# Optimization experiments

Measured on AMD Instinct MI355X. Metric: run time of the kernel, lower is better.

## Reference

```python
import jax, jax.numpy as jnp
import numpy as np
import math

N_NODES = 100000
N_EDGES = 1600000
INPUT_SIZE = 256
N_HEADS = 8
HEAD_SIZE = INPUT_SIZE // N_HEADS  # 32
DK = math.sqrt(HEAD_SIZE)


def setup_inputs() -> dict:
    key = jax.random.key(0)
    k1, k2, k3, k4, k5 = jax.random.split(key, 5)
    X = jax.random.normal(k1, (N_NODES, INPUT_SIZE), dtype=jnp.float32)
    edge_index = jax.random.randint(k2, (2, N_EDGES), 0, N_NODES, dtype=jnp.int64)
    # kaiming_normal (fan_in = input_size) std = sqrt(2/fan_in)
    std = math.sqrt(2.0 / INPUT_SIZE)
    Wq = jax.random.normal(k3, (INPUT_SIZE, HEAD_SIZE), dtype=jnp.float32) * std
    Wk = jax.random.normal(k4, (INPUT_SIZE, HEAD_SIZE), dtype=jnp.float32) * std
    Wv = jax.random.normal(k5, (INPUT_SIZE, HEAD_SIZE), dtype=jnp.float32) * std
    return {"X": X, "edge_index": edge_index, "Wq": Wq, "Wk": Wk, "Wv": Wv}


def reference(X, edge_index, Wq, Wk, Wv):
    N = X.shape[0]
    Q = X @ Wq  # [N, h]
    K = X @ Wk  # [N, h]
    V = X @ Wv  # [N, h]
    src = edge_index[0]  # row index (softmax over dim=1 -> per-src segments)
    dst = edge_index[1]
    # per-edge QK dot, scaled
    scores = jnp.sum(Q[src] * K[dst], axis=-1) / DK  # [E]
    # segment-wise (sparse) softmax over each row
    row_max = jax.ops.segment_max(scores, src, num_segments=N)  # [N]
    ex = jnp.exp(scores - row_max[src])  # [E]
    denom = jax.ops.segment_sum(ex, src, num_segments=N)  # [N]
    alpha = ex / denom[src]  # [E]
    # sparse-mm aggregate of V: out[i] = sum_j alpha_ij * V[j]
    out = jax.ops.segment_sum(alpha[:, None] * V[dst], src, num_segments=N)  # [N, h]
    return out
```

## Files before the change

### kernel.cpp

```cpp
#include <hip/hip_runtime.h>

#define N_INPUT 256
#define HS 32

#define BKT_SHIFT 7
#define BKT_NODES 128
#define NBUCK_MAX 800
#define CAP 2560
#define EPB 2048

typedef __attribute__((ext_vector_type(8))) short bf16x8;
typedef __attribute__((ext_vector_type(4))) float f32x4;
typedef __attribute__((ext_vector_type(8))) unsigned short u16x8;

__device__ __forceinline__ unsigned short f2bf(float f) {
    unsigned u = __float_as_uint(f);
    unsigned r = u + 0x7FFFu + ((u >> 16) & 1u);
    return (unsigned short)(r >> 16);
}
__device__ __forceinline__ float bf2f(unsigned short u) {
    return __uint_as_float((unsigned)u << 16);
}

__global__ void prep_kernel(int* __restrict__ gtail, int nb,
                            const float* __restrict__ Wq,
                            const float* __restrict__ Wk,
                            const float* __restrict__ Wv,
                            uint4* __restrict__ Wp) {
    int t = threadIdx.x;
    if (blockIdx.x == 0) {
        for (int i = t; i < nb; i += 256) gtail[i] = 0;
        return;
    }
    int c = (int)(blockIdx.x - 1) * 256 + t;
    int s = c >> 9;
    int tt = (c >> 6) & 7;
    int L = c & 63;
    const float* wm = (s < 2) ? Wq : (s < 4) ? Wk : Wv;
    const float* wsrc = wm + (size_t)(tt * 32 + (L >> 4) * 8) * HS + (s & 1) * 16 + (L & 15);
    unsigned e0 = f2bf(wsrc[0 * HS]) | ((unsigned)f2bf(wsrc[1 * HS]) << 16);
    unsigned e1 = f2bf(wsrc[2 * HS]) | ((unsigned)f2bf(wsrc[3 * HS]) << 16);
    unsigned e2 = f2bf(wsrc[4 * HS]) | ((unsigned)f2bf(wsrc[5 * HS]) << 16);
    unsigned e3 = f2bf(wsrc[6 * HS]) | ((unsigned)f2bf(wsrc[7 * HS]) << 16);
    Wp[c] = make_uint4(e0, e1, e2, e3);
}

__global__ __launch_bounds__(256) void mega_kernel(
        const float* __restrict__ X, const uint4* __restrict__ Wp,
        const int* __restrict__ src, const int* __restrict__ dst,
        float* __restrict__ Q, unsigned short* __restrict__ KVb,
        int* __restrict__ gtail, uint2* __restrict__ staging,
        int N, int E, int nb, int s1blocks) {
    __shared__ int sh[NBUCK_MAX];
    __shared__ int sbs[NBUCK_MAX];
    int tid = threadIdx.x;
    int idx = (int)blockIdx.x;
    bool is_s1 = (idx % 3 == 0) && (idx / 3 < s1blocks);

    if (is_s1) {
        int e0 = (idx / 3) * EPB;
        for (int i = tid; i < nb; i += 256) sh[i] = 0;
        __syncthreads();
        int ss[8], dd[8], rr[8];
#pragma unroll
        for (int k = 0; k < 8; ++k) {
            int i = e0 + tid + k * 256;
            ss[k] = -1;
            if (i < E) {
                int s = src[i];
                dd[k] = dst[i];
                ss[k] = s;
                rr[k] = atomicAdd(&sh[s >> BKT_SHIFT], 1);
            }
        }
        __syncthreads();
        for (int b = tid; b < nb; b += 256) {
            int c = sh[b];
            sbs[b] = c ? atomicAdd(&gtail[b], c) : 0;
        }
        __syncthreads();
#pragma unroll
        for (int k = 0; k < 8; ++k) {
            if (ss[k] >= 0) {
                int b = ss[k] >> BKT_SHIFT;
                int pos = sbs[b] + rr[k];
                if (pos < CAP)
                    staging[(size_t)b * CAP + pos] =
                        make_uint2((unsigned)ss[k], (unsigned)dd[k]);
            }
        }
        return;
    }

    int bq = idx - min(idx / 3 + 1, s1blocks);
    int wave = tid >> 6;
    int L = tid & 63;
    int quad = L >> 4;
    int lane16 = L & 15;
    int mt = bq * 4 + wave;
    if (mt * 16 >= N) return;

    const float* xrow = X + (size_t)(mt * 16 + lane16) * N_INPUT + quad * 8;
    bf16x8 afrag[8];
#pragma unroll
    for (int t = 0; t < 8; ++t) {
        float4 a0 = *(const float4*)(xrow + t * 32);
        float4 a1 = *(const float4*)(xrow + t * 32 + 4);
        bf16x8 f;
        f[0] = (short)f2bf(a0.x); f[1] = (short)f2bf(a0.y);
        f[2] = (short)f2bf(a0.z); f[3] = (short)f2bf(a0.w);
        f[4] = (short)f2bf(a1.x); f[5] = (short)f2bf(a1.y);
        f[6] = (short)f2bf(a1.z); f[7] = (short)f2bf(a1.w);
        afrag[t] = f;
    }

#pragma unroll
    for (int s = 0; s < 6; ++s) {
        f32x4 acc = {0.f, 0.f, 0.f, 0.f};
#pragma unroll
        for (int t = 0; t < 8; ++t) {
            bf16x8 bfrag = ((const bf16x8*)Wp)[(s * 8 + t) * 64 + L];
            acc = __builtin_amdgcn_mfma_f32_16x16x32_bf16(afrag[t], bfrag, acc, 0, 0, 0);
        }
        int col = (s & 1) * 16 + lane16;
#pragma unroll
        for (int r = 0; r < 4; ++r) {
            int row = mt * 16 + quad * 4 + r;
            if (s < 2) {
                Q[(size_t)row * HS + col] = acc[r];
            } else {
                size_t pos = (size_t)row * 64 + (size_t)(col >> 2) * 8 +
                             ((s < 4) ? 0 : 4) + (col & 3);
                KVb[pos] = f2bf(acc[r]);
            }
        }
    }
}

__global__ __launch_bounds__(512) void s2_agg_kernel(
        const uint2* __restrict__ staging, const int* __restrict__ gtail,
        const float* __restrict__ Q, const unsigned short* __restrict__ KVb,
        float* __restrict__ out, int N) {
    __shared__ int ldst[CAP];
    __shared__ int nh[BKT_NODES];
    __shared__ int nx[BKT_NODES];
    __shared__ int rk[BKT_NODES];
    int b = blockIdx.x;
    int t = threadIdx.x;
    int cnt = min(gtail[b], CAP);
    if (t < BKT_NODES) { nh[t] = 0; rk[t] = 0; }
    __syncthreads();
    uint2 stash[5];
#pragma unroll
    for (int k = 0; k < 5; ++k) {
        int i = t + k * 512;
        if (i < cnt) {
            uint2 e = staging[(size_t)b * CAP + i];
            stash[k] = e;
            atomicAdd(&nh[e.x & (BKT_NODES - 1)], 1);
        }
    }
    __syncthreads();
    if (t < BKT_NODES) nx[t] = nh[t];
    __syncthreads();
    for (int off = 1; off < BKT_NODES; off <<= 1) {
        int u = (t >= off && t < BKT_NODES) ? nx[t - off] : 0;
        __syncthreads();
        if (t < BKT_NODES) nx[t] += u;
        __syncthreads();
    }
#pragma unroll
    for (int k = 0; k < 5; ++k) {
        int i = t + k * 512;
        if (i < cnt) {
            uint2 e = stash[k];
            int sl = (int)(e.x & (BKT_NODES - 1));
            int r = atomicAdd(&rk[sl], 1);
            ldst[nx[sl] - nh[sl] + r] = (int)e.y;
        }
    }
    __syncthreads();

    int lane = t & 31;
    int grp = t >> 5;
    int slot = lane >> 3;
    int sub = lane & 7;
    int node0 = b << BKT_SHIFT;
    for (int ni = grp; ni < BKT_NODES; ni += 16) {
        int n = node0 + ni;
        if (n >= N) continue;
        int end = nx[ni];
        int beg = end - nh[ni];
        float4 qf = *(const float4*)(Q + (size_t)n * HS + sub * 4);
        float4 acc = make_float4(0.f, 0.f, 0.f, 0.f);
        float den = 0.f;
        for (int j = beg; j < end; j += 4) {
            int e = j + slot;
            bool valid = e < end;
            int d = valid ? ldst[e] : 0;
            u16x8 kv = *(const u16x8*)(KVb + (size_t)d * 64 + sub * 8);
            float p = qf.x * bf2f(kv[0]) + qf.y * bf2f(kv[1]) +
                      qf.z * bf2f(kv[2]) + qf.w * bf2f(kv[3]);
            p += __shfl_xor(p, 1, 32);
            p += __shfl_xor(p, 2, 32);
            p += __shfl_xor(p, 4, 32);
            float ex = valid ? __expf(p * 0.17677669529663687f) : 0.f;
            den += ex;
            acc.x += ex * bf2f(kv[4]);
            acc.y += ex * bf2f(kv[5]);
            acc.z += ex * bf2f(kv[6]);
            acc.w += ex * bf2f(kv[7]);
        }
#pragma unroll
        for (int off = 8; off <= 16; off <<= 1) {
            acc.x += __shfl_xor(acc.x, off, 32);
            acc.y += __shfl_xor(acc.y, off, 32);
            acc.z += __shfl_xor(acc.z, off, 32);
            acc.w += __shfl_xor(acc.w, off, 32);
            den += __shfl_xor(den, off, 32);
        }
        if (lane < 8) {
            float4 o = make_float4(0.f, 0.f, 0.f, 0.f);
            if (end > beg) {
                float rd = 1.f / den;
                o = make_float4(acc.x * rd, acc.y * rd, acc.z * rd, acc.w * rd);
            }
            *(float4*)(out + (size_t)n * HS + lane * 4) = o;
        }
    }
}

extern "C" void kernel_launch(void* const* d_in, const int* in_sizes, int n_in,
                              void* d_out, int out_size, void* d_ws, size_t ws_size,
                              hipStream_t stream) {
    const float* X  = (const float*)d_in[0];
    const int*   ei = (const int*)d_in[1];
    const float* Wq = (const float*)d_in[2];
    const float* Wk = (const float*)d_in[3];
    const float* Wv = (const float*)d_in[4];

    int N = in_sizes[0] / N_INPUT;
    int E = in_sizes[1] / 2;
    const int* src = ei;
    const int* dst = ei + E;

    float* ws = (float*)d_ws;
    float* Q = ws;
    unsigned short* KVb = (unsigned short*)(Q + (size_t)N * HS);
    uint4* Wp = (uint4*)(KVb + (size_t)N * 64);
    int* gtail = (int*)(Wp + 3072);
    uint2* staging = (uint2*)(gtail + NBUCK_MAX);
    float* out = (float*)d_out;

    int nbuck = (N + BKT_NODES - 1) >> BKT_SHIFT;
    int s1blocks = (E + EPB - 1) / EPB;
    int mtiles = (N + 15) / 16;
    int qblocks = (mtiles + 3) / 4;

    prep_kernel<<<13, 256, 0, stream>>>(gtail, nbuck, Wq, Wk, Wv, Wp);
    mega_kernel<<<s1blocks + qblocks, 256, 0, stream>>>(
        X, Wp, src, dst, Q, KVb, gtail, staging, N, E, nbuck, s1blocks);
    s2_agg_kernel<<<nbuck, 512, 0, stream>>>(staging, gtail, Q, KVb, out, N);
}
```

Baseline: 231.8 us.

## Pack staged edges into 32-bit words and enlarge binning chunks per block

Staged edges are now packed into one 32-bit word holding the local source slot (7 bits) and the destination index (17 bits) instead of an 8-byte pair. This halves staging write and read traffic between the binning and aggregation stages. Each binning block now processes 16384 edges with a two-pass count-then-scatter loop, which cuts the number of global gtail atomics. The interleave ratio between binning and projection blocks is now computed from the block counts. The cost is that src is read twice and fewer, longer binning blocks may finish late. The packing also limits node indices to 17 bits, which only holds for N up to 131072.

```diff
diff --git a/kernel.cpp b/kernel.cpp
--- a/kernel.cpp
+++ b/kernel.cpp
@@ -7,7 +7,7 @@
 #define BKT_NODES 128
 #define NBUCK_MAX 800
 #define CAP 2560
-#define EPB 2048
+#define EPB 16384
 
 typedef __attribute__((ext_vector_type(8))) short bf16x8;
 typedef __attribute__((ext_vector_type(4))) float f32x4;
@@ -49,50 +49,42 @@
         const float* __restrict__ X, const uint4* __restrict__ Wp,
         const int* __restrict__ src, const int* __restrict__ dst,
         float* __restrict__ Q, unsigned short* __restrict__ KVb,
-        int* __restrict__ gtail, uint2* __restrict__ staging,
-        int N, int E, int nb, int s1blocks) {
+        int* __restrict__ gtail, unsigned* __restrict__ staging,
+        int N, int E, int nb, int s1blocks, int ilv) {
     __shared__ int sh[NBUCK_MAX];
     __shared__ int sbs[NBUCK_MAX];
+    __shared__ int srk[NBUCK_MAX];
     int tid = threadIdx.x;
     int idx = (int)blockIdx.x;
-    bool is_s1 = (idx % 3 == 0) && (idx / 3 < s1blocks);
+    bool is_s1 = (idx % ilv == 0) && (idx / ilv < s1blocks);
 
     if (is_s1) {
-        int e0 = (idx / 3) * EPB;
-        for (int i = tid; i < nb; i += 256) sh[i] = 0;
-        __syncthreads();
-        int ss[8], dd[8], rr[8];
-#pragma unroll
-        for (int k = 0; k < 8; ++k) {
-            int i = e0 + tid + k * 256;
-            ss[k] = -1;
-            if (i < E) {
-                int s = src[i];
-                dd[k] = dst[i];
-                ss[k] = s;
-                rr[k] = atomicAdd(&sh[s >> BKT_SHIFT], 1);
-            }
-        }
+        int e0 = (idx / ilv) * EPB;
+        int lim = min(EPB, E - e0);
+        for (int i = tid; i < nb; i += 256) { sh[i] = 0; srk[i] = 0; }
+        __syncthreads();
+        for (int i = tid; i < lim; i += 256)
+            atomicAdd(&sh[src[e0 + i] >> BKT_SHIFT], 1);
         __syncthreads();
         for (int b = tid; b < nb; b += 256) {
             int c = sh[b];
             sbs[b] = c ? atomicAdd(&gtail[b], c) : 0;
         }
         __syncthreads();
-#pragma unroll
-        for (int k = 0; k < 8; ++k) {
-            if (ss[k] >= 0) {
-                int b = ss[k] >> BKT_SHIFT;
-                int pos = sbs[b] + rr[k];
-                if (pos < CAP)
-                    staging[(size_t)b * CAP + pos] =
-                        make_uint2((unsigned)ss[k], (unsigned)dd[k]);
-            }
+        for (int i = tid; i < lim; i += 256) {
+            int s = src[e0 + i];
+            unsigned d = (unsigned)dst[e0 + i];
+            int b = s >> BKT_SHIFT;
+            int r = atomicAdd(&srk[b], 1);
+            int pos = sbs[b] + r;
+            if (pos < CAP)
+                staging[(size_t)b * CAP + pos] =
+                    ((unsigned)(s & (BKT_NODES - 1)) << 17) | d;
         }
         return;
     }
 
-    int bq = idx - min(idx / 3 + 1, s1blocks);
+    int bq = idx - min(idx / ilv + 1, s1blocks);
     int wave = tid >> 6;
     int L = tid & 63;
     int quad = L >> 4;
@@ -138,7 +130,7 @@
 }
 
 __global__ __launch_bounds__(512) void s2_agg_kernel(
-        const uint2* __restrict__ staging, const int* __restrict__ gtail,
+        const unsigned* __restrict__ staging, const int* __restrict__ gtail,
         const float* __restrict__ Q, const unsigned short* __restrict__ KVb,
         float* __restrict__ out, int N) {
     __shared__ int ldst[CAP];
@@ -150,14 +142,14 @@
     int cnt = min(gtail[b], CAP);
     if (t < BKT_NODES) { nh[t] = 0; rk[t] = 0; }
     __syncthreads();
-    uint2 stash[5];
+    unsigned stash[5];
 #pragma unroll
     for (int k = 0; k < 5; ++k) {
         int i = t + k * 512;
         if (i < cnt) {
-            uint2 e = staging[(size_t)b * CAP + i];
+            unsigned e = staging[(size_t)b * CAP + i];
             stash[k] = e;
-            atomicAdd(&nh[e.x & (BKT_NODES - 1)], 1);
+            atomicAdd(&nh[e >> 17], 1);
         }
     }
     __syncthreads();
@@ -173,10 +165,10 @@
     for (int k = 0; k < 5; ++k) {
         int i = t + k * 512;
         if (i < cnt) {
-            uint2 e = stash[k];
-            int sl = (int)(e.x & (BKT_NODES - 1));
+            unsigned e = stash[k];
+            int sl = (int)(e >> 17);
             int r = atomicAdd(&rk[sl], 1);
-            ldst[nx[sl] - nh[sl] + r] = (int)e.y;
+            ldst[nx[sl] - nh[sl] + r] = (int)(e & 0x1FFFFu);
         }
     }
     __syncthreads();
@@ -249,16 +241,19 @@
     unsigned short* KVb = (unsigned short*)(Q + (size_t)N * HS);
     uint4* Wp = (uint4*)(KVb + (size_t)N * 64);
     int* gtail = (int*)(Wp + 3072);
-    uint2* staging = (uint2*)(gtail + NBUCK_MAX);
+    unsigned* staging = (unsigned*)(gtail + NBUCK_MAX);
     float* out = (float*)d_out;
 
     int nbuck = (N + BKT_NODES - 1) >> BKT_SHIFT;
     int s1blocks = (E + EPB - 1) / EPB;
     int mtiles = (N + 15) / 16;
     int qblocks = (mtiles + 3) / 4;
+    int total = s1blocks + qblocks;
+    int ilv = total / s1blocks;
+    if (ilv < 1) ilv = 1;
 
     prep_kernel<<<13, 256, 0, stream>>>(gtail, nbuck, Wq, Wk, Wv, Wp);
-    mega_kernel<<<s1blocks + qblocks, 256, 0, stream>>>(
-        X, Wp, src, dst, Q, KVb, gtail, staging, N, E, nbuck, s1blocks);
+    mega_kernel<<<total, 256, 0, stream>>>(
+        X, Wp, src, dst, Q, KVb, gtail, staging, N, E, nbuck, s1blocks, ilv);
     s2_agg_kernel<<<nbuck, 512, 0, stream>>>(staging, gtail, Q, KVb, out, N);
 }
```

New measurement: 472.8 us. +103.9%, slower.

## Pack staged edges into 32-bit words and prefetch next KV gather

Applied to the files above, without the earlier changes.

Staging entries drop from a (src,dst) uint2 to a single 32-bit word holding the local source slot (7 bits) and the destination (17 bits). This halves the staging write and read traffic between the bucketing and aggregation kernels. The aggregation loop also software-pipelines the gathered KV load, fetching the next iteration's row while the current one is being computed, to hide gather latency. The packing assumes fewer than 2^17 nodes, and the prefetch adds register pressure.

```diff
diff --git a/kernel.cpp b/kernel.cpp
--- a/kernel.cpp
+++ b/kernel.cpp
@@ -49,7 +49,7 @@
         const float* __restrict__ X, const uint4* __restrict__ Wp,
         const int* __restrict__ src, const int* __restrict__ dst,
         float* __restrict__ Q, unsigned short* __restrict__ KVb,
-        int* __restrict__ gtail, uint2* __restrict__ staging,
+        int* __restrict__ gtail, unsigned* __restrict__ staging,
         int N, int E, int nb, int s1blocks) {
     __shared__ int sh[NBUCK_MAX];
     __shared__ int sbs[NBUCK_MAX];
@@ -86,7 +86,7 @@
                 int pos = sbs[b] + rr[k];
                 if (pos < CAP)
                     staging[(size_t)b * CAP + pos] =
-                        make_uint2((unsigned)ss[k], (unsigned)dd[k]);
+                        ((unsigned)(ss[k] & (BKT_NODES - 1)) << 17) | (unsigned)dd[k];
             }
         }
         return;
@@ -138,7 +138,7 @@
 }
 
 __global__ __launch_bounds__(512) void s2_agg_kernel(
-        const uint2* __restrict__ staging, const int* __restrict__ gtail,
+        const unsigned* __restrict__ staging, const int* __restrict__ gtail,
         const float* __restrict__ Q, const unsigned short* __restrict__ KVb,
         float* __restrict__ out, int N) {
     __shared__ int ldst[CAP];
@@ -150,14 +150,14 @@
     int cnt = min(gtail[b], CAP);
     if (t < BKT_NODES) { nh[t] = 0; rk[t] = 0; }
     __syncthreads();
-    uint2 stash[5];
+    unsigned stash[5];
 #pragma unroll
     for (int k = 0; k < 5; ++k) {
         int i = t + k * 512;
         if (i < cnt) {
-            uint2 e = staging[(size_t)b * CAP + i];
+            unsigned e = staging[(size_t)b * CAP + i];
             stash[k] = e;
-            atomicAdd(&nh[e.x & (BKT_NODES - 1)], 1);
+            atomicAdd(&nh[e >> 17], 1);
         }
     }
     __syncthreads();
@@ -173,10 +173,10 @@
     for (int k = 0; k < 5; ++k) {
         int i = t + k * 512;
         if (i < cnt) {
-            uint2 e = stash[k];
-            int sl = (int)(e.x & (BKT_NODES - 1));
+            unsigned e = stash[k];
+            int sl = (int)(e >> 17);
             int r = atomicAdd(&rk[sl], 1);
-            ldst[nx[sl] - nh[sl] + r] = (int)e.y;
+            ldst[nx[sl] - nh[sl] + r] = (int)(e & 0x1FFFFu);
         }
     }
     __syncthreads();
@@ -194,11 +194,16 @@
         float4 qf = *(const float4*)(Q + (size_t)n * HS + sub * 4);
         float4 acc = make_float4(0.f, 0.f, 0.f, 0.f);
         float den = 0.f;
+        int d0 = (beg + slot < end) ? ldst[beg + slot] : 0;
+        u16x8 kvc = *(const u16x8*)(KVb + (size_t)d0 * 64 + sub * 8);
         for (int j = beg; j < end; j += 4) {
-            int e = j + slot;
-            bool valid = e < end;
-            int d = valid ? ldst[e] : 0;
-            u16x8 kv = *(const u16x8*)(KVb + (size_t)d * 64 + sub * 8);
+            bool valid = (j + slot) < end;
+            u16x8 kv = kvc;
+            int jn = j + 4;
+            if (jn < end) {
+                int dn = (jn + slot < end) ? ldst[jn + slot] : 0;
+                kvc = *(const u16x8*)(KVb + (size_t)dn * 64 + sub * 8);
+            }
             float p = qf.x * bf2f(kv[0]) + qf.y * bf2f(kv[1]) +
                       qf.z * bf2f(kv[2]) + qf.w * bf2f(kv[3]);
             p += __shfl_xor(p, 1, 32);
@@ -249,7 +254,7 @@
     unsigned short* KVb = (unsigned short*)(Q + (size_t)N * HS);
     uint4* Wp = (uint4*)(KVb + (size_t)N * 64);
     int* gtail = (int*)(Wp + 3072);
-    uint2* staging = (uint2*)(gtail + NBUCK_MAX);
+    unsigned* staging = (unsigned*)(gtail + NBUCK_MAX);
     float* out = (float*)d_out;
 
     int nbuck = (N + BKT_NODES - 1) >> BKT_SHIFT;
```

Result: no change. 229.3 us (-1.1%).
